# Kernel optimization log

Hardware: AMD Instinct MI355X
Metric: run time of the kernel (lower is better)

The kernel has to match this reference:

```python
import jax, jax.numpy as jnp
import numpy as np

H = 8  # num_heads
EPS = 1e-5

def _layernorm(x, g, b):
    mu = jnp.mean(x, axis=-1, keepdims=True)
    var = jnp.var(x, axis=-1, keepdims=True)
    return (x - mu) * jax.lax.rsqrt(var + EPS) * g + b

def setup_inputs() -> dict:
    key = jax.random.key(0)
    ks = jax.random.split(key, 16)
    B, S, D, F = 1, 4096, 512, 2048
    s = 1.0 / np.sqrt(D)
    inp = {
        'x': jax.random.normal(ks[0], (B, S, D), jnp.float32),
        'mask': jax.random.randint(ks[1], (S, S), 0, 2, jnp.int32),
        'wq': jax.random.normal(ks[2], (D, D), jnp.float32) * s,
        'bq': jnp.zeros((D,), jnp.float32),
        'wk': jax.random.normal(ks[3], (D, D), jnp.float32) * s,
        'bk': jnp.zeros((D,), jnp.float32),
        'wv': jax.random.normal(ks[4], (D, D), jnp.float32) * s,
        'bv': jnp.zeros((D,), jnp.float32),
        'wo': jax.random.normal(ks[5], (D, D), jnp.float32) * s,
        'bo': jnp.zeros((D,), jnp.float32),
        'w1': jax.random.normal(ks[6], (D, F), jnp.float32) * s,
        'b1': jnp.zeros((F,), jnp.float32),
        'w2': jax.random.normal(ks[7], (F, D), jnp.float32) * (1.0 / np.sqrt(F)),
        'b2': jnp.zeros((D,), jnp.float32),
        'g1': jnp.ones((D,), jnp.float32),
        'be1': jnp.zeros((D,), jnp.float32),
        'g2': jnp.ones((D,), jnp.float32),
        'be2': jnp.zeros((D,), jnp.float32),
    }
    return inp

def reference(x, mask, wq, bq, wk, bk, wv, bv, wo, bo, w1, b1, w2, b2, g1, be1, g2, be2):
    B, S, D = x.shape
    Dh = D // H

    def split(t):  # (B,S,D) -> (B,H,S,Dh)
        return t.reshape(B, S, H, Dh).transpose(0, 2, 1, 3)

    q = split(x @ wq + bq)
    k = split(x @ wk + bk)
    v = split(x @ wv + bv)

    # naive attention: full (B,H,S,S) scores, NO 1/sqrt(Dh) scaling (faithful to source)
    scores = jnp.einsum('bhsd,bhtd->bhst', q, k)
    scores = jnp.where(mask == 0, jnp.float32(-1e9), scores)
    attn = jax.nn.softmax(scores, axis=-1)
    out = jnp.einsum('bhst,bhtd->bhsd', attn, v)
    out = out.transpose(0, 2, 1, 3).reshape(B, S, D) @ wo + bo

    x = _layernorm(x + out, g1, be1)  # dropout is identity at inference
    ff = jax.nn.relu(x @ w1 + b1) @ w2 + b2
    x = _layernorm(x + ff, g2, be2)
    return x
```

## Files before the change

kernel.cpp:

```cpp
#include <hip/hip_runtime.h>

typedef unsigned short u16;
typedef unsigned int u32;
typedef unsigned long long u64;
typedef __attribute__((ext_vector_type(4))) float f32x4;
typedef __attribute__((ext_vector_type(8))) short bf16x8;
typedef __attribute__((ext_vector_type(4))) u16 u16x4;
typedef __attribute__((ext_vector_type(2))) u32 u32x2;

#define DEV __device__ __forceinline__

DEV u16 f2bf(float f) {
  union { float f; u32 u; } c; c.f = f;
  u32 u = c.u;
  u += 0x7fffu + ((u >> 16) & 1u);
  return (u16)(u >> 16);
}
DEV float bf2f(u16 h) {
  union { u32 u; float f; } c; c.u = ((u32)h) << 16;
  return c.f;
}
DEV u32 fbits(float f) { union { float f; u32 u; } c; c.f = f; return c.u; }
DEV u32 packtrunc(float a, float b) {
  return (fbits(b) & 0xFFFF0000u) | (fbits(a) >> 16);
}

DEV void gload_lds16(const void* g, void* l) {
  __builtin_amdgcn_global_load_lds(
      (const __attribute__((address_space(1))) u32*)(u64)g,
      (__attribute__((address_space(3))) u32*)(u32)(u64)l,
      16, 0, 0);
}

struct PrepW { const float* w; u16* th; u16* tl; int R, C, gxmask, gxshift; };
struct PrepArgs {
  const float* x; u16* xh; u16* xl;
  const int* mask; unsigned long long* mbits;
  PrepW pw[6];
};

__global__ __launch_bounds__(256) void prep(PrepArgs a) {
  __shared__ float t[32][33];
  int b = blockIdx.x, tid = threadIdx.x;
  if (b < 2048) {
    int i = (b * 256 + tid) * 4;
    f32x4 v = *(const f32x4*)(a.x + i);
    u16x4 h, l;
#pragma unroll
    for (int j = 0; j < 4; ++j) { h[j] = f2bf(v[j]); l[j] = f2bf(v[j] - bf2f(h[j])); }
    *(u16x4*)(a.xh + i) = h;
    *(u16x4*)(a.xl + i) = l;
    return;
  }
  b -= 2048;
  if (b < 3072) {
    int wi, base;
    if (b < 1024) { wi = b >> 8; base = b & 255; }
    else if (b < 2048) { wi = 4; base = b - 1024; }
    else { wi = 5; base = b - 2048; }
    PrepW p = a.pw[wi];
    int c0 = (base & p.gxmask) * 32, r0 = (base >> p.gxshift) * 32;
    int tx = tid & 31, ty = tid >> 5;
#pragma unroll
    for (int i = 0; i < 4; ++i)
      t[ty + 8 * i][tx] = p.w[(size_t)(r0 + ty + 8 * i) * p.C + c0 + tx];
    __syncthreads();
#pragma unroll
    for (int i = 0; i < 4; ++i) {
      float v = t[tx][ty + 8 * i];
      u16 h = f2bf(v);
      size_t o = (size_t)(c0 + ty + 8 * i) * p.R + r0 + tx;
      p.th[o] = h;
      p.tl[o] = f2bf(v - bf2f(h));
    }
    return;
  }
  b -= 3072;
  size_t i = (size_t)b * 256 + tid;
  unsigned long long bb = __ballot(a.mask[i] != 0);
  if ((tid & 63) == 0) a.mbits[i >> 6] = bb;
}

struct QkvArgs {
  const u16 *Ah, *Al;
  const u16 *Bh[3], *Bl[3];
  const float* bias[3];
  u16 *Qh, *Ql, *Kh, *Vt;
};

__global__ __launch_bounds__(256) void gemm_qkv(QkvArgs a) {
  const int K = 512;
  const float L2E = 1.44269504088896340736f;
  const int z = blockIdx.z;
  const u16* __restrict__ Bh = a.Bh[z];
  const u16* __restrict__ Bl = a.Bl[z];
  const float* __restrict__ bias = a.bias[z];
  const int bn = blockIdx.x * 128, bm = blockIdx.y * 128;
  const int tid = threadIdx.x;
  const int wave = tid >> 6, lane = tid & 63;
  const int l16 = lane & 15, quad = lane >> 4;
  const int wm = (wave >> 1) * 64, wn = (wave & 1) * 64;

  __shared__ u16 sA[128 * 32];
  __shared__ u16 sB[128 * 32];
  __shared__ u16 sAl[128 * 32];
  __shared__ u16 sBl[128 * 32];

  const int srow = wave * 32 + (lane >> 2);
  const int scol = (lane & 3) * 8;
  const u16* srcA0 = a.Ah + (size_t)(bm + srow) * K + scol;
  const u16* srcB0 = Bh + (size_t)(bn + srow) * K + scol;
  const u16* srcAl0 = a.Al + (size_t)(bm + srow) * K + scol;
  const u16* srcBl0 = Bl + (size_t)(bn + srow) * K + scol;
  const size_t half_off = (size_t)16 * K;
  u16* dstA = sA + wave * 1024;
  u16* dstB = sB + wave * 1024;
  u16* dstAl = sAl + wave * 1024;
  u16* dstBl = sBl + wave * 1024;

  f32x4 acc[4][4] = {};

  for (int kt = 0; kt < K; kt += 32) {
    gload_lds16(srcA0 + kt, dstA);
    gload_lds16(srcA0 + half_off + kt, dstA + 512);
    gload_lds16(srcB0 + kt, dstB);
    gload_lds16(srcB0 + half_off + kt, dstB + 512);
    gload_lds16(srcAl0 + kt, dstAl);
    gload_lds16(srcAl0 + half_off + kt, dstAl + 512);
    gload_lds16(srcBl0 + kt, dstBl);
    gload_lds16(srcBl0 + half_off + kt, dstBl + 512);
    __syncthreads();

    bf16x8 a_h[4], b_h[4], a_l[4], b_l[4];
#pragma unroll
    for (int mt = 0; mt < 4; ++mt) {
      a_h[mt] = *(const bf16x8*)(sA + (wm + mt * 16 + l16) * 32 + quad * 8);
      a_l[mt] = *(const bf16x8*)(sAl + (wm + mt * 16 + l16) * 32 + quad * 8);
    }
#pragma unroll
    for (int nt = 0; nt < 4; ++nt) {
      b_h[nt] = *(const bf16x8*)(sB + (wn + nt * 16 + l16) * 32 + quad * 8);
      b_l[nt] = *(const bf16x8*)(sBl + (wn + nt * 16 + l16) * 32 + quad * 8);
    }
#pragma unroll
    for (int mt = 0; mt < 4; ++mt)
#pragma unroll
      for (int nt = 0; nt < 4; ++nt) {
        acc[mt][nt] = __builtin_amdgcn_mfma_f32_16x16x32_bf16(a_h[mt], b_h[nt], acc[mt][nt], 0, 0, 0);
        acc[mt][nt] = __builtin_amdgcn_mfma_f32_16x16x32_bf16(a_h[mt], b_l[nt], acc[mt][nt], 0, 0, 0);
        acc[mt][nt] = __builtin_amdgcn_mfma_f32_16x16x32_bf16(a_l[mt], b_h[nt], acc[mt][nt], 0, 0, 0);
      }
    __syncthreads();
  }

  if (z == 2) {
#pragma unroll
    for (int nt = 0; nt < 4; ++nt) {
      int col = bn + wn + nt * 16 + l16;
      float bv = bias[col];
#pragma unroll
      for (int mt = 0; mt < 4; ++mt) {
        int row0 = bm + wm + mt * 16 + quad * 4;
        u16x4 o;
#pragma unroll
        for (int r = 0; r < 4; ++r) o[r] = f2bf(acc[mt][nt][r] + bv);
        *(u16x4*)(a.Vt + (size_t)col * 4096 + row0) = o;
      }
    }
  } else if (z == 0) {
#pragma unroll
    for (int mt = 0; mt < 4; ++mt)
#pragma unroll
      for (int nt = 0; nt < 4; ++nt) {
        int col = bn + wn + nt * 16 + l16;
        float bv = bias[col];
#pragma unroll
        for (int r = 0; r < 4; ++r) {
          int row = bm + wm + mt * 16 + quad * 4 + r;
          float v = (acc[mt][nt][r] + bv) * L2E;
          u16 h = f2bf(v);
          size_t oidx = (size_t)row * 512 + col;
          a.Qh[oidx] = h;
          a.Ql[oidx] = f2bf(v - bf2f(h));
        }
      }
  } else {
#pragma unroll
    for (int mt = 0; mt < 4; ++mt)
#pragma unroll
      for (int nt = 0; nt < 4; ++nt) {
        int col = bn + wn + nt * 16 + l16;
        float bv = bias[col];
#pragma unroll
        for (int r = 0; r < 4; ++r) {
          int row = bm + wm + mt * 16 + quad * 4 + r;
          a.Kh[(size_t)row * 512 + col] = f2bf(acc[mt][nt][r] + bv);
        }
      }
  }
}

template <int RELU, int BF16OUT>
__global__ __launch_bounds__(256) void gemm_bt(const u16* __restrict__ Ah,
                                               const u16* __restrict__ Bh,
                                               const float* __restrict__ bias,
                                               float* __restrict__ Cf,
                                               u16* __restrict__ Ch,
                                               int N, int K) {
  const int bn = blockIdx.x * 128, bm = blockIdx.y * 128;
  const int tid = threadIdx.x;
  const int wave = tid >> 6, lane = tid & 63;
  const int l16 = lane & 15, quad = lane >> 4;
  const int wm = (wave >> 1) * 64, wn = (wave & 1) * 64;

  __shared__ u16 sA[128 * 32];
  __shared__ u16 sB[128 * 32];

  const int srow = wave * 32 + (lane >> 2);
  const int scol = (lane & 3) * 8;
  const u16* srcA0 = Ah + (size_t)(bm + srow) * K + scol;
  const u16* srcB0 = Bh + (size_t)(bn + srow) * K + scol;
  const size_t half_off = (size_t)16 * K;
  u16* dstA = sA + wave * 1024;
  u16* dstB = sB + wave * 1024;

  f32x4 acc[4][4] = {};

  for (int kt = 0; kt < K; kt += 32) {
    gload_lds16(srcA0 + kt, dstA);
    gload_lds16(srcA0 + half_off + kt, dstA + 512);
    gload_lds16(srcB0 + kt, dstB);
    gload_lds16(srcB0 + half_off + kt, dstB + 512);
    __syncthreads();

    bf16x8 a_h[4], b_h[4];
#pragma unroll
    for (int mt = 0; mt < 4; ++mt)
      a_h[mt] = *(const bf16x8*)(sA + (wm + mt * 16 + l16) * 32 + quad * 8);
#pragma unroll
    for (int nt = 0; nt < 4; ++nt)
      b_h[nt] = *(const bf16x8*)(sB + (wn + nt * 16 + l16) * 32 + quad * 8);
#pragma unroll
    for (int mt = 0; mt < 4; ++mt)
#pragma unroll
      for (int nt = 0; nt < 4; ++nt)
        acc[mt][nt] = __builtin_amdgcn_mfma_f32_16x16x32_bf16(a_h[mt], b_h[nt], acc[mt][nt], 0, 0, 0);
    __syncthreads();
  }

#pragma unroll
  for (int mt = 0; mt < 4; ++mt)
#pragma unroll
    for (int nt = 0; nt < 4; ++nt) {
      int col = bn + wn + nt * 16 + l16;
      float bv = bias ? bias[col] : 0.f;
#pragma unroll
      for (int r = 0; r < 4; ++r) {
        int row = bm + wm + mt * 16 + quad * 4 + r;
        float v = acc[mt][nt][r] + bv;
        if (RELU) v = fmaxf(v, 0.f);
        size_t oidx = (size_t)row * N + col;
        if (BF16OUT) Ch[oidx] = f2bf(v);
        else Cf[oidx] = v;
      }
    }
}

__global__ __launch_bounds__(256) void attn(const u16* __restrict__ Qh, const u16* __restrict__ Ql,
                                            const u16* __restrict__ Kh, const u16* __restrict__ Vt,
                                            const u64* __restrict__ mb64,
                                            float* __restrict__ O0, float* __restrict__ O1,
                                            float* __restrict__ O2, float* __restrict__ O3,
                                            float* __restrict__ lp) {
  const int S = 4096, D = 512;
  const int h = blockIdx.x >> 2, chunk = blockIdx.x & 3;
  const int tid = threadIdx.x, wave = tid >> 6, lane = tid & 63;
  const int l16 = lane & 15, quad = lane >> 4;
  const int q0w = blockIdx.y * 128 + wave * 32;
  const int kbeg = chunk * 1024;
  const int sw = l16 & 7;

  __shared__ u16 sK[64 * 64];
  __shared__ u16 sV[80 * 64];
  __shared__ u16 sP[4][32 * 64];
  u16* myP = &sP[wave][0];

  if (tid < 16) ((u64*)(sV + 64 * 64))[tid] = 0x3F803F803F803F80ULL;
  for (int idx = tid; idx < 240; idx += 256) ((u64*)(sV + 65 * 64))[idx] = 0;

  const int skey = lane >> 3;
  const int sch  = lane & 7;
  const u16* srcK = Kh + (size_t)(kbeg + wave * 8 + skey) * D + h * 64 + ((sch ^ skey) * 8);
  const u16* srcV = Vt + (size_t)(h * 64 + wave * 8 + skey) * S + kbeg + ((sch ^ skey) * 8);
  u16* dstK = sK + wave * 512;
  u16* dstV = sV + wave * 512;

  bf16x8 qfh[2][2], qfl[2][2];
#pragma unroll
  for (int qt = 0; qt < 2; ++qt)
#pragma unroll
    for (int kd = 0; kd < 2; ++kd) {
      size_t qb = (size_t)(q0w + qt * 16 + l16) * D + h * 64 + kd * 32 + quad * 8;
      qfh[qt][kd] = *(const bf16x8*)(Qh + qb);
      qfl[qt][kd] = *(const bf16x8*)(Ql + qb);
    }

  f32x4 accO[2][5] = {};
  const int wbase = kbeg >> 6;

  for (int it = 0; it < 16; ++it) {
    gload_lds16(srcK, dstK);
    gload_lds16(srcK + (size_t)32 * D, dstK + 32 * 64);
    gload_lds16(srcV, dstV);
    gload_lds16(srcV + (size_t)32 * S, dstV + 32 * 64);
    srcK += (size_t)64 * D; srcV += 64;
    __syncthreads();

    u64 wm[2];
#pragma unroll
    for (int qt = 0; qt < 2; ++qt)
      wm[qt] = mb64[(size_t)(q0w + qt * 16 + l16) * 64 + wbase + it];

#pragma unroll
    for (int half = 0; half < 2; ++half) {
      f32x4 sc[2][2];
#pragma unroll
      for (int k2 = 0; k2 < 2; ++k2) {
        const int kt4 = half * 2 + k2;
        const u16* arow = sK + (kt4 * 16 + l16) * 64;
        bf16x8 ka0 = *(const bf16x8*)(arow + ((quad ^ sw) * 8));
        bf16x8 ka1 = *(const bf16x8*)(arow + (((4 + quad) ^ sw) * 8));
#pragma unroll
        for (int qt = 0; qt < 2; ++qt) {
          f32x4 s = {};
          s = __builtin_amdgcn_mfma_f32_16x16x32_bf16(ka0, qfh[qt][0], s, 0, 0, 0);
          s = __builtin_amdgcn_mfma_f32_16x16x32_bf16(ka1, qfh[qt][1], s, 0, 0, 0);
          s = __builtin_amdgcn_mfma_f32_16x16x32_bf16(ka0, qfl[qt][0], s, 0, 0, 0);
          s = __builtin_amdgcn_mfma_f32_16x16x32_bf16(ka1, qfl[qt][1], s, 0, 0, 0);
          sc[k2][qt] = s;
        }
      }
#pragma unroll
      for (int k2 = 0; k2 < 2; ++k2) {
        const int kt4 = half * 2 + k2;
        const int baseb = (kt4 & 1) * 16 + quad * 4;
#pragma unroll
        for (int qt = 0; qt < 2; ++qt) {
          u32 wbits = half ? (u32)(wm[qt] >> 32) : (u32)wm[qt];
          float p[4];
#pragma unroll
          for (int r = 0; r < 4; ++r) {
            bool keep = (wbits >> (baseb + r)) & 1u;
            p[r] = exp2f(keep ? sc[k2][qt][r] : -1e9f);
          }
          int row = qt * 16 + l16;
          int pos = (kt4 * 2 + (quad >> 1)) ^ sw;
          u32x2 pk = {packtrunc(p[0], p[1]), packtrunc(p[2], p[3])};
          *(u32x2*)(myP + row * 64 + pos * 8 + (quad & 1) * 4) = pk;
        }
      }
    }
#pragma unroll
    for (int kt2 = 0; kt2 < 2; ++kt2) {
      bf16x8 pa[2];
#pragma unroll
      for (int qt = 0; qt < 2; ++qt)
        pa[qt] = *(const bf16x8*)(myP + (qt * 16 + l16) * 64 + (((kt2 * 4 + quad) ^ sw) * 8));
#pragma unroll
      for (int nt = 0; nt < 5; ++nt) {
        bf16x8 vf = *(const bf16x8*)(sV + (nt * 16 + l16) * 64 + (((kt2 * 4 + quad) ^ sw) * 8));
#pragma unroll
        for (int qt = 0; qt < 2; ++qt)
          accO[qt][nt] = __builtin_amdgcn_mfma_f32_16x16x32_bf16(pa[qt], vf, accO[qt][nt], 0, 0, 0);
      }
    }
    __syncthreads();
  }

  float* Op = (chunk < 2) ? (chunk ? O1 : O0) : (chunk == 2 ? O2 : O3);
#pragma unroll
  for (int qt = 0; qt < 2; ++qt)
#pragma unroll
    for (int nt = 0; nt < 4; ++nt)
#pragma unroll
      for (int r = 0; r < 4; ++r) {
        int row = q0w + qt * 16 + quad * 4 + r;
        Op[((size_t)h * S + row) * 64 + nt * 16 + l16] = accO[qt][nt][r];
      }
  if (l16 == 0)
#pragma unroll
    for (int qt = 0; qt < 2; ++qt)
#pragma unroll
      for (int r = 0; r < 4; ++r)
        lp[((size_t)h * 4 + chunk) * S + q0w + qt * 16 + quad * 4 + r] = accO[qt][4][r];
}

__global__ __launch_bounds__(256) void attn_combine(const float* __restrict__ O0,
                                                    const float* __restrict__ O1,
                                                    const float* __restrict__ O2,
                                                    const float* __restrict__ O3,
                                                    const float* __restrict__ lp,
                                                    u16* __restrict__ ctx) {
  const int S = 4096;
  int i = (blockIdx.x * 256 + threadIdx.x);
  int row = i >> 7;
  int col4 = (i & 127) * 4;
  int h = col4 >> 6, c = col4 & 63;
  size_t ob = ((size_t)h * S + row) * 64 + c;
  f32x4 o = *(const f32x4*)(O0 + ob) + *(const f32x4*)(O1 + ob) +
            *(const f32x4*)(O2 + ob) + *(const f32x4*)(O3 + ob);
  float l = lp[((size_t)h * 4 + 0) * S + row] + lp[((size_t)h * 4 + 1) * S + row] +
            lp[((size_t)h * 4 + 2) * S + row] + lp[((size_t)h * 4 + 3) * S + row];
  float rl = 1.f / l;
  u16x4 out;
#pragma unroll
  for (int j = 0; j < 4; ++j) out[j] = f2bf(o[j] * rl);
  *(u16x4*)(ctx + (size_t)row * 512 + col4) = out;
}

__global__ __launch_bounds__(256) void resid_ln(const float* __restrict__ X,
                                                const float* __restrict__ Y,
                                                const float* __restrict__ g,
                                                const float* __restrict__ b,
                                                float* __restrict__ outF,
                                                u16* __restrict__ outH) {
  int row = blockIdx.x * 4 + (int)(threadIdx.x >> 6);
  int lane = threadIdx.x & 63;
  const float* x0 = X + (size_t)row * 512;
  const float* y0 = Y + (size_t)row * 512;
  int c0 = lane * 4, c1 = 256 + lane * 4;
  f32x4 v0 = *(const f32x4*)(x0 + c0) + *(const f32x4*)(y0 + c0);
  f32x4 v1 = *(const f32x4*)(x0 + c1) + *(const f32x4*)(y0 + c1);
  float s = 0.f, s2 = 0.f;
#pragma unroll
  for (int j = 0; j < 4; ++j) {
    s += v0[j] + v1[j];
    s2 += v0[j] * v0[j] + v1[j] * v1[j];
  }
#pragma unroll
  for (int m = 1; m < 64; m <<= 1) {
    s += __shfl_xor(s, m);
    s2 += __shfl_xor(s2, m);
  }
  float mean = s * (1.f / 512.f);
  float var = s2 * (1.f / 512.f) - mean * mean;
  float rs = rsqrtf(var + 1e-5f);
  f32x4 o0, o1;
#pragma unroll
  for (int j = 0; j < 4; ++j) {
    o0[j] = (v0[j] - mean) * rs * g[c0 + j] + b[c0 + j];
    o1[j] = (v1[j] - mean) * rs * g[c1 + j] + b[c1 + j];
  }
  if (outF) {
    *(f32x4*)(outF + (size_t)row * 512 + c0) = o0;
    *(f32x4*)(outF + (size_t)row * 512 + c1) = o1;
  }
  if (outH) {
    u16x4 h0, h1;
#pragma unroll
    for (int j = 0; j < 4; ++j) { h0[j] = f2bf(o0[j]); h1[j] = f2bf(o1[j]); }
    *(u16x4*)(outH + (size_t)row * 512 + c0) = h0;
    *(u16x4*)(outH + (size_t)row * 512 + c1) = h1;
  }
}

extern "C" void kernel_launch(void* const* d_in, const int* in_sizes, int n_in,
                              void* d_out, int out_size, void* d_ws, size_t ws_size,
                              hipStream_t stream) {
  (void)in_sizes; (void)n_in; (void)out_size; (void)ws_size;
  const float* x   = (const float*)d_in[0];
  const int*   mask= (const int*)d_in[1];
  const float* wq  = (const float*)d_in[2];
  const float* bq  = (const float*)d_in[3];
  const float* wk  = (const float*)d_in[4];
  const float* bk  = (const float*)d_in[5];
  const float* wv  = (const float*)d_in[6];
  const float* bv  = (const float*)d_in[7];
  const float* wo  = (const float*)d_in[8];
  const float* bo  = (const float*)d_in[9];
  const float* w1  = (const float*)d_in[10];
  const float* b1  = (const float*)d_in[11];
  const float* w2  = (const float*)d_in[12];
  const float* b2  = (const float*)d_in[13];
  const float* g1  = (const float*)d_in[14];
  const float* be1 = (const float*)d_in[15];
  const float* g2  = (const float*)d_in[16];
  const float* be2 = (const float*)d_in[17];

  const int S = 4096, D = 512, F = 2048;
  char* ws = (char*)d_ws;
  size_t cur = 0;
  auto alloc = [&](size_t bytes) {
    char* p = ws + cur;
    cur += (bytes + 255) & ~(size_t)255;
    return p;
  };
  u16* wqT_h = (u16*)alloc((size_t)D * D * 2); u16* wqT_l = (u16*)alloc((size_t)D * D * 2);
  u16* wkT_h = (u16*)alloc((size_t)D * D * 2); u16* wkT_l = (u16*)alloc((size_t)D * D * 2);
  u16* wvT_h = (u16*)alloc((size_t)D * D * 2); u16* wvT_l = (u16*)alloc((size_t)D * D * 2);
  u16* woT_h = (u16*)alloc((size_t)D * D * 2); u16* woT_l = (u16*)alloc((size_t)D * D * 2);
  u16* w1T_h = (u16*)alloc((size_t)D * F * 2); u16* w1T_l = (u16*)alloc((size_t)D * F * 2);
  u16* w2T_h = (u16*)alloc((size_t)D * F * 2); u16* w2T_l = (u16*)alloc((size_t)D * F * 2);
  u32* mbits = (u32*)alloc((size_t)S * S / 8);
  u16* xh = (u16*)alloc((size_t)S * D * 2);
  u16* xl = (u16*)alloc((size_t)S * D * 2);
  u16* Qh = (u16*)alloc((size_t)S * D * 2);
  u16* Ql = (u16*)alloc((size_t)S * D * 2);
  u16* Kh = (u16*)alloc((size_t)S * D * 2);
  u16* Vt = (u16*)alloc((size_t)S * D * 2);
  u16* ctx = (u16*)alloc((size_t)S * D * 2);
  float* x1 = (float*)alloc((size_t)S * D * 4);
  u16* x1h = (u16*)alloc((size_t)S * D * 2);
  float* Oex = (float*)alloc((size_t)2 * S * D * 4);
  float* O0 = (float*)xh;
  float* O1 = x1;
  float* O2 = Oex;
  float* O3 = Oex + (size_t)S * D;
  float* lp = (float*)x1h;
  float* proj = (float*)xh;
  u16* hbuf = Qh;
  float* ff2 = Oex;

  PrepArgs pa;
  pa.x = x; pa.xh = xh; pa.xl = xl;
  pa.mask = mask; pa.mbits = (unsigned long long*)mbits;
  pa.pw[0] = {wq, wqT_h, wqT_l, D, D, 15, 4};
  pa.pw[1] = {wk, wkT_h, wkT_l, D, D, 15, 4};
  pa.pw[2] = {wv, wvT_h, wvT_l, D, D, 15, 4};
  pa.pw[3] = {wo, woT_h, woT_l, D, D, 15, 4};
  pa.pw[4] = {w1, w1T_h, w1T_l, D, F, 63, 6};
  pa.pw[5] = {w2, w2T_h, w2T_l, F, D, 15, 4};

  QkvArgs qa;
  qa.Ah = xh; qa.Al = xl;
  qa.Bh[0] = wqT_h; qa.Bh[1] = wkT_h; qa.Bh[2] = wvT_h;
  qa.Bl[0] = wqT_l; qa.Bl[1] = wkT_l; qa.Bl[2] = wvT_l;
  qa.bias[0] = bq; qa.bias[1] = bk; qa.bias[2] = bv;
  qa.Qh = Qh; qa.Ql = Ql; qa.Kh = Kh; qa.Vt = Vt;

  prep<<<70656, 256, 0, stream>>>(pa);
  gemm_qkv<<<dim3(4, 32, 3), 256, 0, stream>>>(qa);
  attn<<<dim3(32, 32), 256, 0, stream>>>(Qh, Ql, Kh, Vt, (const u64*)mbits, O0, O1, O2, O3, lp);
  attn_combine<<<(S * D / 4) / 256, 256, 0, stream>>>(O0, O1, O2, O3, lp, ctx);
  gemm_bt<0, 0><<<dim3(4, 32), 256, 0, stream>>>(ctx, woT_h, bo, proj, nullptr, D, D);
  resid_ln<<<S / 4, 256, 0, stream>>>(x, proj, g1, be1, x1, x1h);
  gemm_bt<1, 1><<<dim3(16, 32), 256, 0, stream>>>(x1h, w1T_h, b1, nullptr, hbuf, F, D);
  gemm_bt<0, 0><<<dim3(4, 32), 256, 0, stream>>>(hbuf, w2T_h, b2, ff2, nullptr, D, F);
  resid_ln<<<S / 4, 256, 0, stream>>>(x1, ff2, g2, be2, (float*)d_out, nullptr);
}
```

Measured before the change: 370.8 us.

## Double-buffer LDS tiles in GEMM and attention kernels to overlap loads with MFMA

Both the GEMM and the attention kernel now use two LDS buffers. The next K/V (or A/B) tile is issued into the spare buffer right after a single barrier, so the global-to-LDS copy overlaps the current tile's MFMA work, and the trailing barrier is dropped. The attention kernel also fetches the next mask word one iteration early and no longer zeroes the unused padding rows of sV. The cost is more LDS per block (attention goes from about 34KB to about 52KB), which can lower the number of resident blocks per CU.

Measured after the change: 355.2 us. -4.2%, faster.

```diff
diff --git a/kernel.cpp b/kernel.cpp
--- a/kernel.cpp
+++ b/kernel.cpp
@@ -213,39 +213,46 @@
   const int l16 = lane & 15, quad = lane >> 4;
   const int wm = (wave >> 1) * 64, wn = (wave & 1) * 64;
 
-  __shared__ u16 sA[128 * 32];
-  __shared__ u16 sB[128 * 32];
+  __shared__ u16 sA[2][128 * 32];
+  __shared__ u16 sB[2][128 * 32];
 
   const int srow = wave * 32 + (lane >> 2);
   const int scol = (lane & 3) * 8;
   const u16* srcA0 = Ah + (size_t)(bm + srow) * K + scol;
   const u16* srcB0 = Bh + (size_t)(bn + srow) * K + scol;
   const size_t half_off = (size_t)16 * K;
-  u16* dstA = sA + wave * 1024;
-  u16* dstB = sB + wave * 1024;
+
+  auto prefetchG = [&](int kt, int buf) {
+    u16* dA = sA[buf] + wave * 1024;
+    u16* dB = sB[buf] + wave * 1024;
+    gload_lds16(srcA0 + kt, dA);
+    gload_lds16(srcA0 + half_off + kt, dA + 512);
+    gload_lds16(srcB0 + kt, dB);
+    gload_lds16(srcB0 + half_off + kt, dB + 512);
+  };
 
   f32x4 acc[4][4] = {};
-
-  for (int kt = 0; kt < K; kt += 32) {
-    gload_lds16(srcA0 + kt, dstA);
-    gload_lds16(srcA0 + half_off + kt, dstA + 512);
-    gload_lds16(srcB0 + kt, dstB);
-    gload_lds16(srcB0 + half_off + kt, dstB + 512);
+  prefetchG(0, 0);
+
+  const int steps = K >> 5;
+  for (int i = 0; i < steps; ++i) {
     __syncthreads();
+    if (i + 1 < steps) prefetchG((i + 1) << 5, (i + 1) & 1);
+    const u16* bufA = sA[i & 1];
+    const u16* bufB = sB[i & 1];
 
     bf16x8 a_h[4], b_h[4];
 #pragma unroll
     for (int mt = 0; mt < 4; ++mt)
-      a_h[mt] = *(const bf16x8*)(sA + (wm + mt * 16 + l16) * 32 + quad * 8);
+      a_h[mt] = *(const bf16x8*)(bufA + (wm + mt * 16 + l16) * 32 + quad * 8);
 #pragma unroll
     for (int nt = 0; nt < 4; ++nt)
-      b_h[nt] = *(const bf16x8*)(sB + (wn + nt * 16 + l16) * 32 + quad * 8);
+      b_h[nt] = *(const bf16x8*)(bufB + (wn + nt * 16 + l16) * 32 + quad * 8);
 #pragma unroll
     for (int mt = 0; mt < 4; ++mt)
 #pragma unroll
       for (int nt = 0; nt < 4; ++nt)
         acc[mt][nt] = __builtin_amdgcn_mfma_f32_16x16x32_bf16(a_h[mt], b_h[nt], acc[mt][nt], 0, 0, 0);
-    __syncthreads();
   }
 
 #pragma unroll
@@ -280,20 +287,32 @@
   const int kbeg = chunk * 1024;
   const int sw = l16 & 7;
 
-  __shared__ u16 sK[64 * 64];
-  __shared__ u16 sV[80 * 64];
+  __shared__ u16 sK[2][64 * 64];
+  __shared__ u16 sV[2][80 * 64];
   __shared__ u16 sP[4][32 * 64];
   u16* myP = &sP[wave][0];
 
-  if (tid < 16) ((u64*)(sV + 64 * 64))[tid] = 0x3F803F803F803F80ULL;
-  for (int idx = tid; idx < 240; idx += 256) ((u64*)(sV + 65 * 64))[idx] = 0;
+  if (tid < 16) {
+    ((u64*)(sV[0] + 64 * 64))[tid] = 0x3F803F803F803F80ULL;
+    ((u64*)(sV[1] + 64 * 64))[tid] = 0x3F803F803F803F80ULL;
+  }
 
   const int skey = lane >> 3;
   const int sch  = lane & 7;
   const u16* srcK = Kh + (size_t)(kbeg + wave * 8 + skey) * D + h * 64 + ((sch ^ skey) * 8);
   const u16* srcV = Vt + (size_t)(h * 64 + wave * 8 + skey) * S + kbeg + ((sch ^ skey) * 8);
-  u16* dstK = sK + wave * 512;
-  u16* dstV = sV + wave * 512;
+
+  auto prefetchKV = [&](int it) {
+    int buf = it & 1;
+    const u16* pK = srcK + (size_t)it * 64 * D;
+    const u16* pV = srcV + it * 64;
+    u16* dK = sK[buf] + wave * 512;
+    u16* dV = sV[buf] + wave * 512;
+    gload_lds16(pK, dK);
+    gload_lds16(pK + (size_t)32 * D, dK + 32 * 64);
+    gload_lds16(pV, dV);
+    gload_lds16(pV + (size_t)32 * S, dV + 32 * 64);
+  };
 
   bf16x8 qfh[2][2], qfl[2][2];
 #pragma unroll
@@ -308,18 +327,23 @@
   f32x4 accO[2][5] = {};
   const int wbase = kbeg >> 6;
 
+  prefetchKV(0);
+  u64 wmCur[2];
+#pragma unroll
+  for (int qt = 0; qt < 2; ++qt)
+    wmCur[qt] = mb64[(size_t)(q0w + qt * 16 + l16) * 64 + wbase];
+
   for (int it = 0; it < 16; ++it) {
-    gload_lds16(srcK, dstK);
-    gload_lds16(srcK + (size_t)32 * D, dstK + 32 * 64);
-    gload_lds16(srcV, dstV);
-    gload_lds16(srcV + (size_t)32 * S, dstV + 32 * 64);
-    srcK += (size_t)64 * D; srcV += 64;
     __syncthreads();
-
-    u64 wm[2];
-#pragma unroll
-    for (int qt = 0; qt < 2; ++qt)
-      wm[qt] = mb64[(size_t)(q0w + qt * 16 + l16) * 64 + wbase + it];
+    if (it + 1 < 16) prefetchKV(it + 1);
+    u64 wmNext[2] = {0, 0};
+    if (it + 1 < 16) {
+#pragma unroll
+      for (int qt = 0; qt < 2; ++qt)
+        wmNext[qt] = mb64[(size_t)(q0w + qt * 16 + l16) * 64 + wbase + it + 1];
+    }
+    const u16* bK = sK[it & 1];
+    const u16* bV = sV[it & 1];
 
 #pragma unroll
     for (int half = 0; half < 2; ++half) {
@@ -327,7 +351,7 @@
 #pragma unroll
       for (int k2 = 0; k2 < 2; ++k2) {
         const int kt4 = half * 2 + k2;
-        const u16* arow = sK + (kt4 * 16 + l16) * 64;
+        const u16* arow = bK + (kt4 * 16 + l16) * 64;
         bf16x8 ka0 = *(const bf16x8*)(arow + ((quad ^ sw) * 8));
         bf16x8 ka1 = *(const bf16x8*)(arow + (((4 + quad) ^ sw) * 8));
 #pragma unroll
@@ -346,7 +370,7 @@
         const int baseb = (kt4 & 1) * 16 + quad * 4;
 #pragma unroll
         for (int qt = 0; qt < 2; ++qt) {
-          u32 wbits = half ? (u32)(wm[qt] >> 32) : (u32)wm[qt];
+          u32 wbits = half ? (u32)(wmCur[qt] >> 32) : (u32)wmCur[qt];
           float p[4];
 #pragma unroll
           for (int r = 0; r < 4; ++r) {
@@ -368,13 +392,14 @@
         pa[qt] = *(const bf16x8*)(myP + (qt * 16 + l16) * 64 + (((kt2 * 4 + quad) ^ sw) * 8));
 #pragma unroll
       for (int nt = 0; nt < 5; ++nt) {
-        bf16x8 vf = *(const bf16x8*)(sV + (nt * 16 + l16) * 64 + (((kt2 * 4 + quad) ^ sw) * 8));
+        bf16x8 vf = *(const bf16x8*)(bV + (nt * 16 + l16) * 64 + (((kt2 * 4 + quad) ^ sw) * 8));
 #pragma unroll
         for (int qt = 0; qt < 2; ++qt)
           accO[qt][nt] = __builtin_amdgcn_mfma_f32_16x16x32_bf16(pa[qt], vf, accO[qt][nt], 0, 0, 0);
       }
     }
-    __syncthreads();
+    wmCur[0] = wmNext[0];
+    wmCur[1] = wmNext[1];
   }
 
   float* Op = (chunk < 2) ? (chunk ? O1 : O0) : (chunk == 2 ? O2 : O3);
```
